# Optimization experiments

Hardware: AMD Instinct MI355X
Metric: run time of the kernel (lower is better)

The kernel has to match this reference:

```python
import jax, jax.numpy as jnp
import numpy as np

B, N, X, H = 128, 1023, 256, 256  # N = 2**(D+1)-1 perfect binary trees, root at 0


def _lin_init(key, out_d, in_d, scale=None):
    if scale is None:
        scale = 1.0 / np.sqrt(in_d)
    kw, kb = jax.random.split(key)
    W = jax.random.uniform(kw, (out_d, in_d), jnp.float32, -scale, scale)
    b = jax.random.uniform(kb, (out_d,), jnp.float32, -scale, scale)
    return W, b


def setup_inputs() -> dict:
    key = jax.random.key(0)
    ks = jax.random.split(key, 16)
    embed = jax.random.normal(ks[0], (B, N, X), jnp.float32)
    Wf, bf = _lin_init(ks[1], H, X + H)
    Wi, bi = _lin_init(ks[2], H, X + H)
    Wu, bu = _lin_init(ks[3], H, X + H)
    Wo, bo = _lin_init(ks[4], H, X + H)
    # extra nn.Parameter biases, initialized to zeros as in the module
    b_f = jnp.zeros((H,), jnp.float32)
    b_i = jnp.zeros((H,), jnp.float32)
    b_u = jnp.zeros((H,), jnp.float32)
    b_o = jnp.zeros((H,), jnp.float32)
    W1, bl1 = _lin_init(ks[5], H, H)
    W2, bl2 = _lin_init(ks[6], H, H)
    W3, bl3 = _lin_init(ks[7], H, H)
    W4, bl4 = _lin_init(ks[8], H, H)
    return {"embed": embed, "Wf": Wf, "bf": bf, "b_f": b_f, "Wi": Wi, "bi": bi,
            "b_i": b_i, "Wu": Wu, "bu": bu, "b_u": b_u, "Wo": Wo, "bo": bo,
            "b_o": b_o, "W1": W1, "bl1": bl1, "W2": W2, "bl2": bl2,
            "W3": W3, "bl3": bl3, "W4": W4, "bl4": bl4}


def _tree_lstm(embed, Wf, bf, b_f, Wi, bi, b_i, Wu, bu, b_u, Wo, bo, b_o):
    Bn, Nn, Xn = embed.shape
    Hn = Wf.shape[0]
    D = int(np.log2(Nn + 1)) - 1  # leaf level index
    h = jnp.zeros((Bn, Nn, Hn), embed.dtype)
    c = jnp.zeros((Bn, Nn, Hn), embed.dtype)
    # initial (leaf) level: no children -> h_sum = 0, c_tilde = 0 (apply_node_func on init state)
    i_g = jax.nn.sigmoid(bi + b_i)
    u_g = jnp.tanh(bu + b_u)
    c_leaf = i_g * u_g
    h_leaf = jax.nn.sigmoid(bo + b_o) * jnp.tanh(c_leaf)
    ls, lc = 2 ** D - 1, 2 ** D
    h = h.at[:, ls:ls + lc].set(jnp.broadcast_to(h_leaf, (Bn, lc, Hn)))
    c = c.at[:, ls:ls + lc].set(jnp.broadcast_to(c_leaf, (Bn, lc, Hn)))
    # level-by-level leaf->root; children of node n are 2n+1, 2n+2 (contiguous per level)
    for l in range(D - 1, -1, -1):
        s, cnt = 2 ** l - 1, 2 ** l
        cs, ccnt = 2 ** (l + 1) - 1, 2 ** (l + 1)
        ch_h = h[:, cs:cs + ccnt]        # [B, 2*cnt, H]
        ch_c = c[:, cs:cs + ccnt]
        ch_e = embed[:, cs:cs + ccnt]
        # message: cat([h, embed]); reduce: sum over the 2 children
        msg = jnp.concatenate([ch_h, ch_e], axis=-1).reshape(Bn, cnt, 2, Hn + Xn)
        h_sum = msg.sum(axis=2)                                   # [B, cnt, H+X]
        c_sum = ch_c.reshape(Bn, cnt, 2, Hn).sum(axis=2)          # [B, cnt, H]
        f = jax.nn.sigmoid(h_sum @ Wf.T + bf + b_f)
        c_tilde = f * c_sum  # f broadcast over children: f*(c1+c2) == sum_k f*c_k
        i_gate = jax.nn.sigmoid(h_sum @ Wi.T + bi + b_i)
        u = jnp.tanh(h_sum @ Wu.T + bu + b_u)
        c_new = i_gate * u + c_tilde
        o = jax.nn.sigmoid(h_sum @ Wo.T + bo + b_o)
        h_new = o * jnp.tanh(c_new)
        h = h.at[:, s:s + cnt].set(h_new)
        c = c.at[:, s:s + cnt].set(c_new)
    return h[:, 0]  # root hidden state, [B, H]


def reference(embed, Wf, bf, b_f, Wi, bi, b_i, Wu, bu, b_u, Wo, bo, b_o,
              W1, bl1, W2, bl2, W3, bl3, W4, bl4):
    hr = _tree_lstm(embed, Wf, bf, b_f, Wi, bi, b_i, Wu, bu, b_u, Wo, bo, b_o)
    # dropout is identity in eval mode
    y = jnp.tanh(hr @ W1.T + bl1)
    y2 = jax.nn.relu(hr @ W2.T + bl2) @ W3.T + bl3
    return jax.nn.relu((y + y2) @ W4.T + bl4)
```

## Files before the change

### kernel.cpp

```cpp
#include <hip/hip_runtime.h>

#define HD 256
#define KD 512

typedef _Float16 half8 __attribute__((ext_vector_type(8)));
typedef _Float16 half2v __attribute__((ext_vector_type(2)));
typedef _Float16 half4v __attribute__((ext_vector_type(4)));
typedef float floatx4 __attribute__((ext_vector_type(4)));
typedef float floatx2 __attribute__((ext_vector_type(2)));

__device__ __forceinline__ float sigmf_(float x) { return 1.f / (1.f + __expf(-x)); }
__device__ __forceinline__ float tanhf_(float x) {
  x = fminf(fmaxf(x, -15.f), 15.f);
  float e = __expf(2.f * x);
  return (e - 1.f) / (e + 1.f);
}

__global__ void prep_kernel(const float* __restrict__ bf_, const float* __restrict__ b_f,
                            const float* __restrict__ bi_, const float* __restrict__ b_i,
                            const float* __restrict__ bu_, const float* __restrict__ b_u,
                            const float* __restrict__ bo_, const float* __restrict__ b_o,
                            const float* __restrict__ Wf, const float* __restrict__ Wi,
                            const float* __restrict__ Wu, const float* __restrict__ Wo,
                            float* __restrict__ bsum, float* __restrict__ bias2,
                            float* __restrict__ cleaf2)
{
  __shared__ float hl2[HD];
  __shared__ float part[64][4];
  const int t = threadIdx.x;
  float sf = bf_[t] + b_f[t];
  float si = bi_[t] + b_i[t];
  float su = bu_[t] + b_u[t];
  float so = bo_[t] + b_o[t];
  float ig = 1.f / (1.f + expf(-si));
  float uu = tanhf(su);
  float cl = ig * uu;
  float hl = (1.f / (1.f + expf(-so))) * tanhf(cl);
  hl2[t] = 2.f * hl;
  if (blockIdx.x == 0) {
    bsum[t] = sf; bsum[HD + t] = si; bsum[2 * HD + t] = su; bsum[3 * HD + t] = so;
    cleaf2[t] = cl + cl;
  }
  __syncthreads();
  const int g = blockIdx.x >> 2, q = blockIdx.x & 3;
  const int nl = t >> 2, kq = t & 3;
  const float* Wg = (g == 0) ? Wf : (g == 1) ? Wi : (g == 2) ? Wu : Wo;
  const float* w = Wg + (long)(q * 64 + nl) * KD + kq * 64;
  float s = 0.f;
  for (int k = 0; k < 64; k += 4) {
    floatx4 wv = *(const floatx4*)(w + k);
    floatx4 hv = *(const floatx4*)(&hl2[kq * 64 + k]);
    s += wv[0] * hv[0] + wv[1] * hv[1] + wv[2] * hv[2] + wv[3] * hv[3];
  }
  part[nl][kq] = s;
  __syncthreads();
  if (kq == 0) {
    const int n = q * 64 + nl;
    float tot = part[nl][0] + part[nl][1] + part[nl][2] + part[nl][3];
    float bg = (g == 0) ? (bf_[n] + b_f[n]) : (g == 1) ? (bi_[n] + b_i[n])
             : (g == 2) ? (bu_[n] + b_u[n]) : (bo_[n] + b_o[n]);
    bias2[g * HD + n] = bg + tot;
  }
}

__global__ void wcvt_kernel(const float* __restrict__ Wf, const float* __restrict__ Wi,
                            const float* __restrict__ Wu, const float* __restrict__ Wo,
                            _Float16* __restrict__ Wh)
{
  int idx = (blockIdx.x * 256 + threadIdx.x) * 4;
  int g = idx >> 17;
  int rem = idx & ((1 << 17) - 1);
  const float* src = (g == 0) ? Wf : (g == 1) ? Wi : (g == 2) ? Wu : Wo;
  floatx4 v = *(const floatx4*)(src + rem);
  half4v o;
  o[0] = (_Float16)v[0]; o[1] = (_Float16)v[1]; o[2] = (_Float16)v[2]; o[3] = (_Float16)v[3];
  *(half4v*)(Wh + idx) = o;
}

__global__ void esum_kernel(const float* __restrict__ embed, _Float16* __restrict__ esum)
{
  const int task = blockIdx.x * 256 + threadIdx.x;
  if (task >= 511 * 32) return;
  const int b = blockIdx.y;
  const int p = task >> 5, g8 = task & 31;
  const float* e0 = embed + ((long)b * 1023 + 2 * p + 1) * 256 + g8 * 8;
  const float* e1 = e0 + 256;
  floatx4 x0 = *(const floatx4*)(e0);
  floatx4 x1 = *(const floatx4*)(e0 + 4);
  floatx4 y0 = *(const floatx4*)(e1);
  floatx4 y1 = *(const floatx4*)(e1 + 4);
  half8 s;
#pragma unroll
  for (int e = 0; e < 4; ++e) { s[e] = (_Float16)(x0[e] + y0[e]); s[4 + e] = (_Float16)(x1[e] + y1[e]); }
  *(half8*)(esum + ((long)b * 511 + p) * 256 + g8 * 8) = s;
}

__global__ __launch_bounds__(256, 2)
void level_kernel(const _Float16* __restrict__ hsum_in,
                  const float* __restrict__ csum_in,
                  const _Float16* __restrict__ esum,
                  const _Float16* __restrict__ Wh,
                  const float* __restrict__ bias,
                  _Float16* __restrict__ hsum_out,
                  float* __restrict__ csum_out,
                  int l, int leaf, int fin)
{
  __shared__ _Float16 As[128][256];

  const int cb = blockIdx.x;
  const int m0 = blockIdx.y * 128;
  const int t = threadIdx.x;
  const int wave = t >> 6;
  const int lane = t & 63;
  const int lm = lane & 15;
  const int quad = lane >> 4;
  const int rh = wave >> 1;
  const int ch = wave & 1;
  const int ncol = cb * 32 + ch * 16 + lm;

  floatx4 acc[4][4] = {};

  const int srow0 = t >> 3;
  const int sg = t & 7;

  const _Float16* wb = Wh + (long)ncol * KD + quad * 8;

  auto gemm_chunk = [&](int kbase) {
    half8 bcur[4], bnxt[4];
#pragma unroll
    for (int g = 0; g < 4; ++g)
      bcur[g] = *(const half8*)(wb + (long)g * HD * KD + kbase);
#pragma unroll
    for (int ks = 0; ks < 8; ++ks) {
      if (ks < 7) {
#pragma unroll
        for (int g = 0; g < 4; ++g)
          bnxt[g] = *(const half8*)(wb + (long)g * HD * KD + kbase + (ks + 1) * 32);
      }
      half8 afr[4];
#pragma unroll
      for (int mt = 0; mt < 4; ++mt) {
        int row = rh * 64 + mt * 16 + lm;
        afr[mt] = *(const half8*)(&As[row][(((ks * 4 + quad) ^ (row & 7)) * 8)]);
      }
#pragma unroll
      for (int mt = 0; mt < 4; ++mt)
#pragma unroll
        for (int g = 0; g < 4; ++g)
          acc[mt][g] = __builtin_amdgcn_mfma_f32_16x16x32_f16(afr[mt], bcur[g], acc[mt][g], 0, 0, 0);
#pragma unroll
      for (int g = 0; g < 4; ++g) bcur[g] = bnxt[g];
    }
  };

  const int msk = (1 << l) - 1;

  if (!leaf) {
#pragma unroll
    for (int p = 0; p < 4; ++p) {
      const int r = srow0 + 32 * p;
      const _Float16* src = hsum_in + (long)(m0 + r) * HD;
#pragma unroll
      for (int q = 0; q < 4; ++q) {
        int g8 = sg + 8 * q;
        *(half8*)(&As[r][((g8 ^ (r & 7)) * 8)]) = *(const half8*)(src + g8 * 8);
      }
    }
    __syncthreads();
    gemm_chunk(0);
    __syncthreads();
  }

  {
#pragma unroll
    for (int p = 0; p < 4; ++p) {
      const int r = srow0 + 32 * p;
      const int sm = m0 + r;
      const long erow = (long)(sm >> l) * 511 + msk + (sm & msk);
      const _Float16* src = esum + erow * HD;
#pragma unroll
      for (int q = 0; q < 4; ++q) {
        int g8 = sg + 8 * q;
        *(half8*)(&As[r][((g8 ^ (r & 7)) * 8)]) = *(const half8*)(src + g8 * 8);
      }
    }
  }
  __syncthreads();
  gemm_chunk(256);

  const float b0 = bias[ncol];
  const float b1 = bias[HD + ncol];
  const float b2 = bias[2 * HD + ncol];
  const float b3 = bias[3 * HD + ncol];
  const float clv = leaf ? csum_in[ncol] : 0.f;

#pragma unroll
  for (int mt = 0; mt < 4; ++mt) {
    const int mg0 = m0 + rh * 64 + mt * 16 + quad * 4;
    float hv[4], cvv[4];
#pragma unroll
    for (int e = 0; e < 4; ++e) {
      float cs = leaf ? clv : csum_in[(long)(mg0 + e) * HD + ncol];
      float zf = acc[mt][0][e] + b0;
      float zi = acc[mt][1][e] + b1;
      float zu = acc[mt][2][e] + b2;
      float zo = acc[mt][3][e] + b3;
      float f = sigmf_(zf), ig = sigmf_(zi), uu = tanhf_(zu), oo = sigmf_(zo);
      float cn = ig * uu + f * cs;
      cvv[e] = cn;
      hv[e] = oo * tanhf_(cn);
    }
    if (fin) {
#pragma unroll
      for (int e = 0; e < 4; ++e)
        hsum_out[(long)(mg0 + e) * HD + ncol] = (_Float16)hv[e];
    } else {
      const long pr = mg0 >> 1;
      hsum_out[pr * HD + ncol] = (_Float16)(hv[0] + hv[1]);
      hsum_out[(pr + 1) * HD + ncol] = (_Float16)(hv[2] + hv[3]);
      csum_out[pr * HD + ncol] = cvv[0] + cvv[1];
      csum_out[(pr + 1) * HD + ncol] = cvv[2] + cvv[3];
    }
  }
}

__global__ void head_all_kernel(const _Float16* __restrict__ hr,
                                const float* __restrict__ W1, const float* __restrict__ bl1,
                                const float* __restrict__ W2, const float* __restrict__ bl2,
                                const float* __restrict__ W3, const float* __restrict__ bl3,
                                const float* __restrict__ W4, const float* __restrict__ bl4,
                                float* __restrict__ out)
{
  __shared__ float a[HD];
  __shared__ float t1s[HD];
  __shared__ float t2s[HD];
  int b = blockIdx.x, n = threadIdx.x;
  a[n] = (float)hr[b * HD + n];
  __syncthreads();
  {
    const float* w1 = W1 + n * HD;
    const float* w2 = W2 + n * HD;
    float s1 = bl1[n], s2 = bl2[n];
    for (int k = 0; k < HD; k += 4) {
      floatx4 av = *(const floatx4*)(&a[k]);
      floatx4 w1v = *(const floatx4*)(w1 + k);
      floatx4 w2v = *(const floatx4*)(w2 + k);
#pragma unroll
      for (int e = 0; e < 4; ++e) { s1 += av[e] * w1v[e]; s2 += av[e] * w2v[e]; }
    }
    t1s[n] = tanhf_(s1);
    t2s[n] = fmaxf(s2, 0.f);
  }
  __syncthreads();
  {
    const float* w3 = W3 + n * HD;
    float s3 = bl3[n];
    for (int k = 0; k < HD; k += 4) {
      floatx4 av = *(const floatx4*)(&t2s[k]);
      floatx4 wv = *(const floatx4*)(w3 + k);
#pragma unroll
      for (int e = 0; e < 4; ++e) s3 += av[e] * wv[e];
    }
    __syncthreads();
    a[n] = t1s[n] + s3;
  }
  __syncthreads();
  {
    const float* w4 = W4 + n * HD;
    float s4 = bl4[n];
    for (int k = 0; k < HD; k += 4) {
      floatx4 av = *(const floatx4*)(&a[k]);
      floatx4 wv = *(const floatx4*)(w4 + k);
#pragma unroll
      for (int e = 0; e < 4; ++e) s4 += av[e] * wv[e];
    }
    out[b * HD + n] = fmaxf(s4, 0.f);
  }
}

extern "C" void kernel_launch(void* const* d_in, const int* in_sizes, int n_in,
                              void* d_out, int out_size, void* d_ws, size_t ws_size,
                              hipStream_t stream)
{
  (void)in_sizes; (void)n_in; (void)out_size; (void)ws_size;
  const float* embed = (const float*)d_in[0];
  const float* Wf  = (const float*)d_in[1];
  const float* bf_ = (const float*)d_in[2];
  const float* b_f = (const float*)d_in[3];
  const float* Wi  = (const float*)d_in[4];
  const float* bi_ = (const float*)d_in[5];
  const float* b_i = (const float*)d_in[6];
  const float* Wu  = (const float*)d_in[7];
  const float* bu_ = (const float*)d_in[8];
  const float* b_u = (const float*)d_in[9];
  const float* Wo  = (const float*)d_in[10];
  const float* bo_ = (const float*)d_in[11];
  const float* b_o = (const float*)d_in[12];
  const float* W1  = (const float*)d_in[13];
  const float* bl1 = (const float*)d_in[14];
  const float* W2  = (const float*)d_in[15];
  const float* bl2 = (const float*)d_in[16];
  const float* W3  = (const float*)d_in[17];
  const float* bl3 = (const float*)d_in[18];
  const float* W4  = (const float*)d_in[19];
  const float* bl4 = (const float*)d_in[20];

  char* ws = (char*)d_ws;
  _Float16* Wh   = (_Float16*)(ws);
  float* bsum    = (float*)(ws + 1048576);
  float* bias2   = (float*)(ws + 1052672);
  float* cleaf2  = (float*)(ws + 1056768);
  _Float16* hr   = (_Float16*)(ws + 1057792);
  _Float16* esum = (_Float16*)(ws + 1123328);
  _Float16* HsA  = (_Float16*)(ws + 34612224);
  float* CsA     = (float*)(ws + 43000832);
  _Float16* HsB  = (_Float16*)(ws + 59778048);
  float* CsB     = (float*)(ws + 63972352);

  prep_kernel<<<dim3(16), dim3(256), 0, stream>>>(bf_, b_f, bi_, b_i, bu_, b_u, bo_, b_o,
                                                  Wf, Wi, Wu, Wo, bsum, bias2, cleaf2);
  wcvt_kernel<<<dim3(512), dim3(256), 0, stream>>>(Wf, Wi, Wu, Wo, Wh);
  esum_kernel<<<dim3(64, 128), dim3(256), 0, stream>>>(embed, esum);

  _Float16* hbufs[2] = {HsA, HsB};
  float* cbufs[2] = {CsA, CsB};
  int pp = 0;
  const _Float16* hin = nullptr;
  const float* cin = cleaf2;
  for (int l = 8; l >= 0; --l) {
    const int leaf = (l == 8);
    const int fin = (l == 0);
    _Float16* hout = fin ? hr : hbufs[pp];
    float* cout = cbufs[pp];
    dim3 grid(8, 1 << l);
    level_kernel<<<grid, dim3(256), 0, stream>>>(hin, cin, esum, Wh,
                                                 leaf ? bias2 : bsum,
                                                 hout, cout, l, leaf, fin);
    hin = hbufs[pp];
    cin = cbufs[pp];
    pp ^= 1;
  }

  head_all_kernel<<<dim3(128), dim3(256), 0, stream>>>(hr, W1, bl1, W2, bl2, W3, bl3,
                                                       W4, bl4, (float*)d_out);
}
```

Measured before the change: 510.0 us.

## Halve LDS tile to 128-wide K chunks, raise occupancy, swap grid axes

The level kernel now stages the A operand in 128-column K chunks (32 KB LDS instead of 64 KB), looping over 4 chunks (2 for the leaf level) with a continuous B-fragment prefetch across chunk boundaries. Launch bounds rise from 2 to 4 blocks per CU to exploit the smaller LDS footprint. The grid is transposed so consecutive blocks share the same weight column block and walk along rows. The trade is more barriers per block and tighter register limits, which could cause spills.

Result: slower. 562.6 us (+10.3%).

```diff
diff --git a/kernel.cpp b/kernel.cpp
--- a/kernel.cpp
+++ b/kernel.cpp
@@ -95,7 +95,7 @@
   *(half8*)(esum + ((long)b * 511 + p) * 256 + g8 * 8) = s;
 }
 
-__global__ __launch_bounds__(256, 2)
+__global__ __launch_bounds__(256, 4)
 void level_kernel(const _Float16* __restrict__ hsum_in,
                   const float* __restrict__ csum_in,
                   const _Float16* __restrict__ esum,
@@ -105,10 +105,10 @@
                   float* __restrict__ csum_out,
                   int l, int leaf, int fin)
 {
-  __shared__ _Float16 As[128][256];
-
-  const int cb = blockIdx.x;
-  const int m0 = blockIdx.y * 128;
+  __shared__ _Float16 As[128 * 128];
+
+  const int cb = blockIdx.y;
+  const int m0 = blockIdx.x * 128;
   const int t = threadIdx.x;
   const int wave = t >> 6;
   const int lane = t & 63;
@@ -124,69 +124,65 @@
   const int sg = t & 7;
 
   const _Float16* wb = Wh + (long)ncol * KD + quad * 8;
-
-  auto gemm_chunk = [&](int kbase) {
-    half8 bcur[4], bnxt[4];
+  const int msk = (1 << l) - 1;
+
+  const int ck0 = leaf ? 2 : 0;
+  const int nck = leaf ? 2 : 4;
+  const int nks = nck * 4;
+
+  half8 bcur[4], bnxt[4];
+  {
+    const int kof = ck0 * 128;
 #pragma unroll
     for (int g = 0; g < 4; ++g)
-      bcur[g] = *(const half8*)(wb + (long)g * HD * KD + kbase);
-#pragma unroll
-    for (int ks = 0; ks < 8; ++ks) {
-      if (ks < 7) {
-#pragma unroll
-        for (int g = 0; g < 4; ++g)
-          bnxt[g] = *(const half8*)(wb + (long)g * HD * KD + kbase + (ks + 1) * 32);
-      }
-      half8 afr[4];
-#pragma unroll
-      for (int mt = 0; mt < 4; ++mt) {
-        int row = rh * 64 + mt * 16 + lm;
-        afr[mt] = *(const half8*)(&As[row][(((ks * 4 + quad) ^ (row & 7)) * 8)]);
-      }
-#pragma unroll
-      for (int mt = 0; mt < 4; ++mt)
-#pragma unroll
-        for (int g = 0; g < 4; ++g)
-          acc[mt][g] = __builtin_amdgcn_mfma_f32_16x16x32_f16(afr[mt], bcur[g], acc[mt][g], 0, 0, 0);
-#pragma unroll
-      for (int g = 0; g < 4; ++g) bcur[g] = bnxt[g];
-    }
-  };
-
-  const int msk = (1 << l) - 1;
-
-  if (!leaf) {
-#pragma unroll
-    for (int p = 0; p < 4; ++p) {
-      const int r = srow0 + 32 * p;
-      const _Float16* src = hsum_in + (long)(m0 + r) * HD;
-#pragma unroll
-      for (int q = 0; q < 4; ++q) {
-        int g8 = sg + 8 * q;
-        *(half8*)(&As[r][((g8 ^ (r & 7)) * 8)]) = *(const half8*)(src + g8 * 8);
-      }
-    }
-    __syncthreads();
-    gemm_chunk(0);
-    __syncthreads();
-  }
-
-  {
+      bcur[g] = *(const half8*)(wb + (long)g * HD * KD + kof);
+  }
+
+  for (int ci = 0; ci < nck; ++ci) {
+    const int ck = ck0 + ci;
+    const int kk = ck & 1;
 #pragma unroll
     for (int p = 0; p < 4; ++p) {
       const int r = srow0 + 32 * p;
       const int sm = m0 + r;
-      const long erow = (long)(sm >> l) * 511 + msk + (sm & msk);
-      const _Float16* src = esum + erow * HD;
-#pragma unroll
-      for (int q = 0; q < 4; ++q) {
-        int g8 = sg + 8 * q;
-        *(half8*)(&As[r][((g8 ^ (r & 7)) * 8)]) = *(const half8*)(src + g8 * 8);
+      const _Float16* src;
+      if (ck < 2) {
+        src = hsum_in + (long)sm * HD + kk * 128;
+      } else {
+        const long erow = (long)(sm >> l) * 511 + msk + (sm & msk);
+        src = esum + erow * HD + kk * 128;
       }
-    }
-  }
-  __syncthreads();
-  gemm_chunk(256);
+#pragma unroll
+      for (int q = 0; q < 2; ++q) {
+        const int g8 = sg + 8 * q;
+        *(half8*)(&As[r * 128 + ((g8 ^ (r & 7)) * 8)]) = *(const half8*)(src + g8 * 8);
+      }
+    }
+    __syncthreads();
+#pragma unroll
+    for (int ksl = 0; ksl < 4; ++ksl) {
+      const int ksf = ci * 4 + ksl;
+      const int nxt = (ksf + 1 < nks) ? ksf + 1 : 0;
+      const int kofn = (ck0 + (nxt >> 2)) * 128 + (nxt & 3) * 32;
+#pragma unroll
+      for (int g = 0; g < 4; ++g)
+        bnxt[g] = *(const half8*)(wb + (long)g * HD * KD + kofn);
+      half8 afr[4];
+#pragma unroll
+      for (int mt = 0; mt < 4; ++mt) {
+        const int row = rh * 64 + mt * 16 + lm;
+        afr[mt] = *(const half8*)(&As[row * 128 + (((ksl * 4 + quad) ^ (row & 7)) * 8)]);
+      }
+#pragma unroll
+      for (int mt = 0; mt < 4; ++mt)
+#pragma unroll
+        for (int g = 0; g < 4; ++g)
+          acc[mt][g] = __builtin_amdgcn_mfma_f32_16x16x32_f16(afr[mt], bcur[g], acc[mt][g], 0, 0, 0);
+#pragma unroll
+      for (int g = 0; g < 4; ++g) bcur[g] = bnxt[g];
+    }
+    __syncthreads();
+  }
 
   const float b0 = bias[ncol];
   const float b1 = bias[HD + ncol];
@@ -332,7 +328,7 @@
     const int fin = (l == 0);
     _Float16* hout = fin ? hr : hbufs[pp];
     float* cout = cbufs[pp];
-    dim3 grid(8, 1 << l);
+    dim3 grid(1 << l, 8);
     level_kernel<<<grid, dim3(256), 0, stream>>>(hin, cin, esum, Wh,
                                                  leaf ? bias2 : bsum,
                                                  hout, cout, l, leaf, fin);
```

## Load A fragments directly from global memory instead of staging in LDS

Applied to the files above, without the earlier changes.

The level GEMM kernel no longer stages the hsum/esum row tiles through a 64KB shared-memory buffer with __syncthreads. Each wave now loads its MFMA A fragments straight from global memory, double-buffered the same way as the weight fragments. The grid is also transposed so consecutive blocks share the same weight column block and walk different row tiles. This removes the LDS footprint and barriers, which may allow more occupancy. The cost is redundant global/L2 reads of A rows, since both column-half waves now read the same rows.

After: 600.6 us. +17.7%, slower.

```diff
diff --git a/kernel.cpp b/kernel.cpp
--- a/kernel.cpp
+++ b/kernel.cpp
@@ -4,10 +4,8 @@
 #define KD 512
 
 typedef _Float16 half8 __attribute__((ext_vector_type(8)));
-typedef _Float16 half2v __attribute__((ext_vector_type(2)));
 typedef _Float16 half4v __attribute__((ext_vector_type(4)));
 typedef float floatx4 __attribute__((ext_vector_type(4)));
-typedef float floatx2 __attribute__((ext_vector_type(2)));
 
 __device__ __forceinline__ float sigmf_(float x) { return 1.f / (1.f + __expf(-x)); }
 __device__ __forceinline__ float tanhf_(float x) {
@@ -105,10 +103,8 @@
                   float* __restrict__ csum_out,
                   int l, int leaf, int fin)
 {
-  __shared__ _Float16 As[128][256];
-
-  const int cb = blockIdx.x;
-  const int m0 = blockIdx.y * 128;
+  const int cb = blockIdx.y;
+  const int m0 = blockIdx.x * 128;
   const int t = threadIdx.x;
   const int wave = t >> 6;
   const int lane = t & 63;
@@ -120,73 +116,51 @@
 
   floatx4 acc[4][4] = {};
 
-  const int srow0 = t >> 3;
-  const int sg = t & 7;
-
   const _Float16* wb = Wh + (long)ncol * KD + quad * 8;
-
-  auto gemm_chunk = [&](int kbase) {
-    half8 bcur[4], bnxt[4];
+  const int msk = (1 << l) - 1;
+
+  const _Float16* ah[4];
+  const _Float16* ae[4];
+#pragma unroll
+  for (int mt = 0; mt < 4; ++mt) {
+    const int sm = m0 + rh * 64 + mt * 16 + lm;
+    const long erow = (long)(sm >> l) * 511 + msk + (sm & msk);
+    ae[mt] = esum + erow * HD + quad * 8;
+    ah[mt] = leaf ? ae[mt] : (hsum_in + (long)sm * HD + quad * 8);
+  }
+
+  auto gemm8 = [&](const _Float16* const* a, int bk0) {
+    half8 bcur[4], bnxt[4], acur[4], anxt[4];
 #pragma unroll
     for (int g = 0; g < 4; ++g)
-      bcur[g] = *(const half8*)(wb + (long)g * HD * KD + kbase);
+      bcur[g] = *(const half8*)(wb + (long)g * HD * KD + bk0);
+#pragma unroll
+    for (int mt = 0; mt < 4; ++mt)
+      acur[mt] = *(const half8*)(a[mt]);
 #pragma unroll
     for (int ks = 0; ks < 8; ++ks) {
       if (ks < 7) {
 #pragma unroll
         for (int g = 0; g < 4; ++g)
-          bnxt[g] = *(const half8*)(wb + (long)g * HD * KD + kbase + (ks + 1) * 32);
+          bnxt[g] = *(const half8*)(wb + (long)g * HD * KD + bk0 + (ks + 1) * 32);
+#pragma unroll
+        for (int mt = 0; mt < 4; ++mt)
+          anxt[mt] = *(const half8*)(a[mt] + (ks + 1) * 32);
       }
-      half8 afr[4];
-#pragma unroll
-      for (int mt = 0; mt < 4; ++mt) {
-        int row = rh * 64 + mt * 16 + lm;
-        afr[mt] = *(const half8*)(&As[row][(((ks * 4 + quad) ^ (row & 7)) * 8)]);
-      }
 #pragma unroll
       for (int mt = 0; mt < 4; ++mt)
 #pragma unroll
         for (int g = 0; g < 4; ++g)
-          acc[mt][g] = __builtin_amdgcn_mfma_f32_16x16x32_f16(afr[mt], bcur[g], acc[mt][g], 0, 0, 0);
+          acc[mt][g] = __builtin_amdgcn_mfma_f32_16x16x32_f16(acur[mt], bcur[g], acc[mt][g], 0, 0, 0);
 #pragma unroll
       for (int g = 0; g < 4; ++g) bcur[g] = bnxt[g];
+#pragma unroll
+      for (int mt = 0; mt < 4; ++mt) acur[mt] = anxt[mt];
     }
   };
 
-  const int msk = (1 << l) - 1;
-
-  if (!leaf) {
-#pragma unroll
-    for (int p = 0; p < 4; ++p) {
-      const int r = srow0 + 32 * p;
-      const _Float16* src = hsum_in + (long)(m0 + r) * HD;
-#pragma unroll
-      for (int q = 0; q < 4; ++q) {
-        int g8 = sg + 8 * q;
-        *(half8*)(&As[r][((g8 ^ (r & 7)) * 8)]) = *(const half8*)(src + g8 * 8);
-      }
-    }
-    __syncthreads();
-    gemm_chunk(0);
-    __syncthreads();
-  }
-
-  {
-#pragma unroll
-    for (int p = 0; p < 4; ++p) {
-      const int r = srow0 + 32 * p;
-      const int sm = m0 + r;
-      const long erow = (long)(sm >> l) * 511 + msk + (sm & msk);
-      const _Float16* src = esum + erow * HD;
-#pragma unroll
-      for (int q = 0; q < 4; ++q) {
-        int g8 = sg + 8 * q;
-        *(half8*)(&As[r][((g8 ^ (r & 7)) * 8)]) = *(const half8*)(src + g8 * 8);
-      }
-    }
-  }
-  __syncthreads();
-  gemm_chunk(256);
+  if (!leaf) gemm8(ah, 0);
+  gemm8(ae, 256);
 
   const float b0 = bias[ncol];
   const float b1 = bias[HD + ncol];
@@ -332,7 +306,7 @@
     const int fin = (l == 0);
     _Float16* hout = fin ? hr : hbufs[pp];
     float* cout = cbufs[pp];
-    dim3 grid(8, 1 << l);
+    dim3 grid(1 << l, 8);
     level_kernel<<<grid, dim3(256), 0, stream>>>(hin, cin, esum, Wh,
                                                  leaf ? bias2 : bsum,
                                                  hout, cout, l, leaf, fin);
```
